# Kernel tuning notes

Hardware: AMD Instinct MI355X
Metric: run time of the kernel (lower is better)

Reference implementation:

```python
import jax, jax.numpy as jnp
import numpy as np

N_QUBITS = 4
DIM = 2 ** N_QUBITS  # 16
N_PATCH = 14 * 14    # 196 patches of 2x2 on a 28x28 image
NUM_CLASSES = 10


def setup_inputs() -> dict:
    key = jax.random.key(0)
    kx, kw, kb, ku = jax.random.split(key, 4)
    B = 8192
    x = jax.random.uniform(kx, (B, 1, 28, 28), dtype=jnp.float32)
    # RandomLayer (8 random 2-qubit gates) composed into one fixed 16x16 real
    # orthogonal unitary (real because RY encoding + real-parameter gates).
    rng = np.random.default_rng(0)
    A = rng.standard_normal((DIM, DIM)).astype(np.float32)
    Q, _ = np.linalg.qr(A)
    U = jnp.asarray(Q, dtype=jnp.float32)
    W = jax.random.normal(kw, (NUM_CLASSES, N_PATCH * N_QUBITS), dtype=jnp.float32) * 0.02
    b = jax.random.normal(kb, (NUM_CLASSES,), dtype=jnp.float32) * 0.02
    return {"x": x, "U": U, "W": W, "b": b}


def _quanv_features(x, U):
    B = x.shape[0]
    # extract 2x2 patches in row-major order: data = [x[r,c], x[r,c+1], x[r+1,c], x[r+1,c+1]]
    p = x.reshape(B, 14, 2, 14, 2).transpose(0, 1, 3, 2, 4).reshape(B, N_PATCH, 4)
    half = 0.5 * p
    a = jnp.stack([jnp.cos(half), jnp.sin(half)], axis=-1)  # (B,P,4,2): RY(theta)|0>
    # product state over 4 qubits -> statevector (B,P,16), wire 0 = most significant
    state = jnp.einsum('bpi,bpj,bpk,bpl->bpijkl',
                       a[:, :, 0], a[:, :, 1], a[:, :, 2], a[:, :, 3]).reshape(B, N_PATCH, DIM)
    state = jnp.einsum('bpd,ed->bpe', state, U)  # apply random-layer unitary
    probs = state * state                          # (B,P,16), real amplitudes
    # PauliZ expectation per wire: sign (+1/-1) of each qubit bit in basis index
    bits = (jnp.arange(DIM)[:, None] >> jnp.arange(N_QUBITS - 1, -1, -1)[None, :]) & 1
    zsign = (1.0 - 2.0 * bits).astype(jnp.float32)  # (16,4)
    meas = probs @ zsign                             # (B,P,4)
    return meas.reshape(B, N_PATCH * N_QUBITS)       # patch-major, qubit-minor (matches torch.cat)


def reference(x, U, W, b):
    feat = _quanv_features(x, U)
    logits = feat @ W.T + b
    return jax.nn.log_softmax(logits, axis=-1)
```

## Files before the change

kernel.cpp:

```cpp
#include <hip/hip_runtime.h>

typedef __attribute__((ext_vector_type(8))) short short8;
typedef __attribute__((ext_vector_type(4))) float f32x4;

#define THREADS 256
#define WPB 4
#define N_PATCH 196
#define NCLS 10
#define FEAT 784
#define ROWSH 40

union I4S8 { int i[4]; short8 v; };

__global__ __launch_bounds__(THREADS)
void quanv_mfma_kernel(const float* __restrict__ x,
                       const float* __restrict__ U,
                       const float* __restrict__ W,
                       const float* __restrict__ b,
                       float* __restrict__ out, int n_img)
{
    __shared__ unsigned short sB[WPB][64][ROWSH];
    __shared__ float sLog[WPB][16];

    const int t    = threadIdx.x;
    const int w    = t >> 6;
    const int lane = t & 63;
    const int img  = blockIdx.x * WPB + w;
    if (img >= n_img) return;

    const int colc = lane & 15;
    const int kb   = lane >> 4;
    const float sgn0 = (kb & 2) ? -1.f : 1.f;
    const float sgn1 = (kb & 1) ? -1.f : 1.f;
    const int cbase = (kb < 2) ? 3 * kb : (6 + 2 * (kb - 2));
    const int ccnt  = (kb < 2) ? 3 : 2;

    short8 a1, a2;
    {
        const float* Urow = U + colc * 16 + (kb & 1) * 8;
        unsigned ub[8]; float uf[8];
#pragma unroll
        for (int i = 0; i < 8; ++i) { uf[i] = Urow[i]; ub[i] = __float_as_uint(uf[i]); }
        I4S8 hi, lo;
#pragma unroll
        for (int j = 0; j < 4; ++j)
            hi.i[j] = (int)__builtin_amdgcn_perm(ub[2*j+1], ub[2*j], 0x07060302u);
#pragma unroll
        for (int j = 0; j < 4; ++j) {
            unsigned lb0 = __float_as_uint(uf[2*j]   - __uint_as_float(ub[2*j]   & 0xffff0000u));
            unsigned lb1 = __float_as_uint(uf[2*j+1] - __uint_as_float(ub[2*j+1] & 0xffff0000u));
            lo.i[j] = (kb < 2) ? (int)__builtin_amdgcn_perm(lb1, lb0, 0x07060302u) : 0;
        }
        a1 = hi.v; a2 = lo.v;
    }

    const float* ximg = x + (size_t)img * FEAT;

    float accl[3] = {0.f, 0.f, 0.f};

    float2 top, bot;
    {
        const int r = lane / 14, cl = lane - r * 14;
        const float* px = ximg + r * 56 + cl * 2;
        top = *(const float2*)px;
        bot = *(const float2*)(px + 28);
    }

#pragma unroll 1
    for (int it = 0; it < 4; ++it) {
        float2 ntop = top, nbot = bot;
        if (it < 3) {
            const int pmn = (it + 1) * 64 + lane;
            const int pcn = (pmn < N_PATCH) ? pmn : N_PATCH - 1;
            const int r = pcn / 14, cl = pcn - r * 14;
            const float* px = ximg + r * 56 + cl * 2;
            ntop = *(const float2*)px;
            nbot = *(const float2*)(px + 28);
        }

        const bool vld = (it * 64 + lane < N_PATCH);

        const float c0 = __cosf(0.5f * top.x), s0 = __sinf(0.5f * top.x);
        const float c1 = __cosf(0.5f * top.y), s1 = __sinf(0.5f * top.y);
        const float c2 = __cosf(0.5f * bot.x), s2 = __sinf(0.5f * bot.x);
        const float c3 = __cosf(0.5f * bot.y), s3 = __sinf(0.5f * bot.y);

        const float wm = vld ? 1.f : 0.f;
        const float p00 = wm * c0 * c1, p01 = wm * c0 * s1;
        const float p10 = wm * s0 * c1, p11 = wm * s0 * s1;
        const float q00 = c2 * c3, q01 = c2 * s3, q10 = s2 * c3, q11 = s2 * s3;
        float st[16];
        st[ 0]=p00*q00; st[ 1]=p00*q01; st[ 2]=p00*q10; st[ 3]=p00*q11;
        st[ 4]=p01*q00; st[ 5]=p01*q01; st[ 6]=p01*q10; st[ 7]=p01*q11;
        st[ 8]=p10*q00; st[ 9]=p10*q01; st[10]=p10*q10; st[11]=p10*q11;
        st[12]=p11*q00; st[13]=p11*q01; st[14]=p11*q10; st[15]=p11*q11;

        I4S8 h0, h1, l0, l1;
#pragma unroll
        for (int j = 0; j < 8; ++j) {
            const unsigned b0 = __float_as_uint(st[2*j]);
            const unsigned b1 = __float_as_uint(st[2*j+1]);
            const unsigned hp = __builtin_amdgcn_perm(b1, b0, 0x07060302u);
            const unsigned lb0 = __float_as_uint(st[2*j]   - __uint_as_float(b0 & 0xffff0000u));
            const unsigned lb1 = __float_as_uint(st[2*j+1] - __uint_as_float(b1 & 0xffff0000u));
            const unsigned lp = __builtin_amdgcn_perm(lb1, lb0, 0x07060302u);
            if (j < 4) { h0.i[j] = (int)hp; l0.i[j] = (int)lp; }
            else       { h1.i[j-4] = (int)hp; l1.i[j-4] = (int)lp; }
        }
        *(short8*)&sB[w][lane][ 0] = h0.v;
        *(short8*)&sB[w][lane][ 8] = h1.v;
        *(short8*)&sB[w][lane][16] = l0.v;
        *(short8*)&sB[w][lane][24] = l1.v;

        const short8 bf0 = *(const short8*)&sB[w][ 0 + colc][8 * kb];
        const short8 bf1 = *(const short8*)&sB[w][16 + colc][8 * kb];
        const short8 bf2 = *(const short8*)&sB[w][32 + colc][8 * kb];
        const short8 bf3 = *(const short8*)&sB[w][48 + colc][8 * kb];

        f32x4 v0 = {0.f,0.f,0.f,0.f}, v1 = v0, v2 = v0, v3 = v0;
        v0 = __builtin_amdgcn_mfma_f32_16x16x32_bf16(a1, bf0, v0, 0, 0, 0);
        v1 = __builtin_amdgcn_mfma_f32_16x16x32_bf16(a1, bf1, v1, 0, 0, 0);
        v2 = __builtin_amdgcn_mfma_f32_16x16x32_bf16(a1, bf2, v2, 0, 0, 0);
        v3 = __builtin_amdgcn_mfma_f32_16x16x32_bf16(a1, bf3, v3, 0, 0, 0);
        v0 = __builtin_amdgcn_mfma_f32_16x16x32_bf16(a2, bf0, v0, 0, 0, 0);
        v1 = __builtin_amdgcn_mfma_f32_16x16x32_bf16(a2, bf1, v1, 0, 0, 0);
        v2 = __builtin_amdgcn_mfma_f32_16x16x32_bf16(a2, bf2, v2, 0, 0, 0);
        v3 = __builtin_amdgcn_mfma_f32_16x16x32_bf16(a2, bf3, v3, 0, 0, 0);

#pragma unroll
        for (int g = 0; g < 4; ++g) {
            const f32x4 amv = (g == 0) ? v0 : (g == 1) ? v1 : (g == 2) ? v2 : v3;
            const float sq0 = amv[0]*amv[0], sq1 = amv[1]*amv[1];
            const float sq2 = amv[2]*amv[2], sq3 = amv[3]*amv[3];
            const float t01 = sq0 + sq1, t23 = sq2 + sq3, sall = t01 + t23;
            float m0 = sgn0 * sall;
            float m1 = sgn1 * sall;
            float m2 = t01 - t23;
            float m3 = (sq0 - sq1) + (sq2 - sq3);

            m0 += __shfl_xor(m0, 16, 64); m0 += __shfl_xor(m0, 32, 64);
            m1 += __shfl_xor(m1, 16, 64); m1 += __shfl_xor(m1, 32, 64);
            m2 += __shfl_xor(m2, 16, 64); m2 += __shfl_xor(m2, 32, 64);
            m3 += __shfl_xor(m3, 16, 64); m3 += __shfl_xor(m3, 32, 64);

            const int pg  = it * 64 + 16 * g + colc;
            const int pcl = (pg < N_PATCH) ? pg : N_PATCH - 1;
#pragma unroll
            for (int cc = 0; cc < 3; ++cc) {
                const int  c     = cbase + cc;
                const bool cval  = (cc < ccnt);
                const int  cSafe = (c < NCLS) ? c : NCLS - 1;
                const float4 wv = *(const float4*)&W[cSafe * FEAT + 4 * pcl];
                const float contrib = m0*wv.x + m1*wv.y + m2*wv.z + m3*wv.w;
                accl[cc] += cval ? contrib : 0.f;
            }
        }

        top = ntop; bot = nbot;
    }

#pragma unroll
    for (int cc = 0; cc < 3; ++cc) {
        float v = accl[cc];
        v += __shfl_xor(v, 1, 64);
        v += __shfl_xor(v, 2, 64);
        v += __shfl_xor(v, 4, 64);
        v += __shfl_xor(v, 8, 64);
        accl[cc] = v;
    }

    if (colc == 0) {
#pragma unroll
        for (int cc = 0; cc < 3; ++cc)
            if (cc < ccnt) sLog[w][cbase + cc] = accl[cc] + b[cbase + cc];
    }
    asm volatile("s_waitcnt lgkmcnt(0)" ::: "memory");

    float lg[NCLS];
#pragma unroll
    for (int c = 0; c < NCLS; ++c) lg[c] = sLog[w][c];

    float m = lg[0];
#pragma unroll
    for (int c = 1; c < NCLS; ++c) m = fmaxf(m, lg[c]);
    float ssum = 0.f;
#pragma unroll
    for (int c = 0; c < NCLS; ++c) ssum += __expf(lg[c] - m);
    const float ls = __logf(ssum);

    if (lane < NCLS)
        out[(size_t)img * NCLS + lane] = lg[lane] - m - ls;
}

extern "C" void kernel_launch(void* const* d_in, const int* in_sizes, int n_in,
                              void* d_out, int out_size, void* d_ws, size_t ws_size,
                              hipStream_t stream) {
    const float* x = (const float*)d_in[0];
    const float* U = (const float*)d_in[1];
    const float* W = (const float*)d_in[2];
    const float* b = (const float*)d_in[3];
    float* out = (float*)d_out;

    const int n_img = in_sizes[0] / FEAT;
    const int grid  = (n_img + WPB - 1) / WPB;

    quanv_mfma_kernel<<<grid, THREADS, 0, stream>>>(x, U, W, b, out, n_img);
}
```

Before: 92.36 us.

## Double-buffer packed state in LDS and use raw v_sin/v_cos

Splits the per-iteration state build into a helper and software-pipelines it. The state for the next 64-patch chunk is computed and written to a second LDS buffer while the MFMA and epilogue work on the current chunk, and input loads are prefetched two chunks ahead. This is meant to hide LDS write-read latency and overlap VALU with MFMA. It also replaces __sinf/__cosf with direct v_sin_f32/v_cos_f32 inline asm, which may lose some accuracy, and doubles the LDS per warp.

```diff
diff --git a/kernel.cpp b/kernel.cpp
--- a/kernel.cpp
+++ b/kernel.cpp
@@ -11,6 +11,53 @@
 #define ROWSH 40
 
 union I4S8 { int i[4]; short8 v; };
+
+__device__ __forceinline__ float fast_sin(float h) {
+    float r = h * 0.15915494309189535f, o;
+    asm("v_sin_f32 %0, %1" : "=v"(o) : "v"(r));
+    return o;
+}
+__device__ __forceinline__ float fast_cos(float h) {
+    float r = h * 0.15915494309189535f, o;
+    asm("v_cos_f32 %0, %1" : "=v"(o) : "v"(r));
+    return o;
+}
+
+__device__ __forceinline__ void pack_store(unsigned short* rowp,
+                                           float2 top, float2 bot, bool vld)
+{
+    const float c0 = fast_cos(0.5f * top.x), s0 = fast_sin(0.5f * top.x);
+    const float c1 = fast_cos(0.5f * top.y), s1 = fast_sin(0.5f * top.y);
+    const float c2 = fast_cos(0.5f * bot.x), s2 = fast_sin(0.5f * bot.x);
+    const float c3 = fast_cos(0.5f * bot.y), s3 = fast_sin(0.5f * bot.y);
+
+    const float wm = vld ? 1.f : 0.f;
+    const float p00 = wm * c0 * c1, p01 = wm * c0 * s1;
+    const float p10 = wm * s0 * c1, p11 = wm * s0 * s1;
+    const float q00 = c2 * c3, q01 = c2 * s3, q10 = s2 * c3, q11 = s2 * s3;
+    float st[16];
+    st[ 0]=p00*q00; st[ 1]=p00*q01; st[ 2]=p00*q10; st[ 3]=p00*q11;
+    st[ 4]=p01*q00; st[ 5]=p01*q01; st[ 6]=p01*q10; st[ 7]=p01*q11;
+    st[ 8]=p10*q00; st[ 9]=p10*q01; st[10]=p10*q10; st[11]=p10*q11;
+    st[12]=p11*q00; st[13]=p11*q01; st[14]=p11*q10; st[15]=p11*q11;
+
+    I4S8 h0, h1, l0, l1;
+#pragma unroll
+    for (int j = 0; j < 8; ++j) {
+        const unsigned b0 = __float_as_uint(st[2*j]);
+        const unsigned b1 = __float_as_uint(st[2*j+1]);
+        const unsigned hp = __builtin_amdgcn_perm(b1, b0, 0x07060302u);
+        const unsigned lb0 = __float_as_uint(st[2*j]   - __uint_as_float(b0 & 0xffff0000u));
+        const unsigned lb1 = __float_as_uint(st[2*j+1] - __uint_as_float(b1 & 0xffff0000u));
+        const unsigned lp = __builtin_amdgcn_perm(lb1, lb0, 0x07060302u);
+        if (j < 4) { h0.i[j] = (int)hp; l0.i[j] = (int)lp; }
+        else       { h1.i[j-4] = (int)hp; l1.i[j-4] = (int)lp; }
+    }
+    *(short8*)(rowp +  0) = h0.v;
+    *(short8*)(rowp +  8) = h1.v;
+    *(short8*)(rowp + 16) = l0.v;
+    *(short8*)(rowp + 24) = l1.v;
+}
 
 __global__ __launch_bounds__(THREADS)
 void quanv_mfma_kernel(const float* __restrict__ x,
@@ -19,7 +66,7 @@
                        const float* __restrict__ b,
                        float* __restrict__ out, int n_img)
 {
-    __shared__ unsigned short sB[WPB][64][ROWSH];
+    __shared__ unsigned short sB[WPB][2][64][ROWSH];
     __shared__ float sLog[WPB][16];
 
     const int t    = threadIdx.x;
@@ -65,57 +112,36 @@
         top = *(const float2*)px;
         bot = *(const float2*)(px + 28);
     }
+    pack_store(&sB[w][0][lane][0], top, bot, true);
+    {
+        const int pmn = 64 + lane;
+        const int r = pmn / 14, cl = pmn - r * 14;
+        const float* px = ximg + r * 56 + cl * 2;
+        top = *(const float2*)px;
+        bot = *(const float2*)(px + 28);
+    }
 
 #pragma unroll 1
     for (int it = 0; it < 4; ++it) {
-        float2 ntop = top, nbot = bot;
+        const int cur = it & 1;
+
         if (it < 3) {
-            const int pmn = (it + 1) * 64 + lane;
-            const int pcn = (pmn < N_PATCH) ? pmn : N_PATCH - 1;
-            const int r = pcn / 14, cl = pcn - r * 14;
-            const float* px = ximg + r * 56 + cl * 2;
-            ntop = *(const float2*)px;
-            nbot = *(const float2*)(px + 28);
+            pack_store(&sB[w][cur ^ 1][lane][0], top, bot,
+                       (it + 1) * 64 + lane < N_PATCH);
+            if (it < 2) {
+                const int pmn = (it + 2) * 64 + lane;
+                const int pcn = (pmn < N_PATCH) ? pmn : N_PATCH - 1;
+                const int r = pcn / 14, cl = pcn - r * 14;
+                const float* px = ximg + r * 56 + cl * 2;
+                top = *(const float2*)px;
+                bot = *(const float2*)(px + 28);
+            }
         }
 
-        const bool vld = (it * 64 + lane < N_PATCH);
-
-        const float c0 = __cosf(0.5f * top.x), s0 = __sinf(0.5f * top.x);
-        const float c1 = __cosf(0.5f * top.y), s1 = __sinf(0.5f * top.y);
-        const float c2 = __cosf(0.5f * bot.x), s2 = __sinf(0.5f * bot.x);
-        const float c3 = __cosf(0.5f * bot.y), s3 = __sinf(0.5f * bot.y);
-
-        const float wm = vld ? 1.f : 0.f;
-        const float p00 = wm * c0 * c1, p01 = wm * c0 * s1;
-        const float p10 = wm * s0 * c1, p11 = wm * s0 * s1;
-        const float q00 = c2 * c3, q01 = c2 * s3, q10 = s2 * c3, q11 = s2 * s3;
-        float st[16];
-        st[ 0]=p00*q00; st[ 1]=p00*q01; st[ 2]=p00*q10; st[ 3]=p00*q11;
-        st[ 4]=p01*q00; st[ 5]=p01*q01; st[ 6]=p01*q10; st[ 7]=p01*q11;
-        st[ 8]=p10*q00; st[ 9]=p10*q01; st[10]=p10*q10; st[11]=p10*q11;
-        st[12]=p11*q00; st[13]=p11*q01; st[14]=p11*q10; st[15]=p11*q11;
-
-        I4S8 h0, h1, l0, l1;
-#pragma unroll
-        for (int j = 0; j < 8; ++j) {
-            const unsigned b0 = __float_as_uint(st[2*j]);
-            const unsigned b1 = __float_as_uint(st[2*j+1]);
-            const unsigned hp = __builtin_amdgcn_perm(b1, b0, 0x07060302u);
-            const unsigned lb0 = __float_as_uint(st[2*j]   - __uint_as_float(b0 & 0xffff0000u));
-            const unsigned lb1 = __float_as_uint(st[2*j+1] - __uint_as_float(b1 & 0xffff0000u));
-            const unsigned lp = __builtin_amdgcn_perm(lb1, lb0, 0x07060302u);
-            if (j < 4) { h0.i[j] = (int)hp; l0.i[j] = (int)lp; }
-            else       { h1.i[j-4] = (int)hp; l1.i[j-4] = (int)lp; }
-        }
-        *(short8*)&sB[w][lane][ 0] = h0.v;
-        *(short8*)&sB[w][lane][ 8] = h1.v;
-        *(short8*)&sB[w][lane][16] = l0.v;
-        *(short8*)&sB[w][lane][24] = l1.v;
-
-        const short8 bf0 = *(const short8*)&sB[w][ 0 + colc][8 * kb];
-        const short8 bf1 = *(const short8*)&sB[w][16 + colc][8 * kb];
-        const short8 bf2 = *(const short8*)&sB[w][32 + colc][8 * kb];
-        const short8 bf3 = *(const short8*)&sB[w][48 + colc][8 * kb];
+        const short8 bf0 = *(const short8*)&sB[w][cur][ 0 + colc][8 * kb];
+        const short8 bf1 = *(const short8*)&sB[w][cur][16 + colc][8 * kb];
+        const short8 bf2 = *(const short8*)&sB[w][cur][32 + colc][8 * kb];
+        const short8 bf3 = *(const short8*)&sB[w][cur][48 + colc][8 * kb];
 
         f32x4 v0 = {0.f,0.f,0.f,0.f}, v1 = v0, v2 = v0, v3 = v0;
         v0 = __builtin_amdgcn_mfma_f32_16x16x32_bf16(a1, bf0, v0, 0, 0, 0);
@@ -155,8 +181,6 @@
                 accl[cc] += cval ? contrib : 0.f;
             }
         }
-
-        top = ntop; bot = nbot;
     }
 
 #pragma unroll
```

Result: no change. 93.45 us (+1.2%).
